# Optimization experiments

Hardware: AMD Instinct MI355X
Metric: run time of the kernel (lower is better)

The kernel has to match this reference:

```python
import jax, jax.numpy as jnp
import numpy as np

STRIDE, PAD, DIL, DG, GROUPS = 1, 1, 1, 1, 1


def setup_inputs() -> dict:
    key = jax.random.key(0)
    k1, k2, k3, k4 = jax.random.split(key, 4)
    B, Cin, H, W = 4, 64, 128, 128
    Cout, kh, kw = 64, 3, 3
    x = jax.random.normal(k1, (B, Cin, H, W), jnp.float32)
    # learned offsets: [B, dg*2*kh*kw, Ho, Wo], interleaved (y, x) per kernel tap
    offset = jax.random.normal(k2, (B, DG * 2 * kh * kw, H, W), jnp.float32)
    # modulation mask: [B, dg*kh*kw, Ho, Wo] in (0,1) (sigmoid applied upstream in DCNv2 packs)
    mask = jax.random.uniform(k3, (B, DG * kh * kw, H, W), jnp.float32)
    stdv = 1.0 / np.sqrt(Cin * kh * kw)
    weight = jax.random.uniform(k4, (Cout, Cin // GROUPS, kh, kw), jnp.float32, -stdv, stdv)
    bias = jnp.zeros((Cout,), jnp.float32)
    return {"x": x, "offset": offset, "mask": mask, "weight": weight, "bias": bias}


def reference(x, offset, mask, weight, bias):
    B, Cin, H, W = x.shape
    Cout, _, kh, kw = weight.shape
    K2 = kh * kw
    Ho = (H + 2 * PAD - DIL * (kh - 1) - 1) // STRIDE + 1
    Wo = (W + 2 * PAD - DIL * (kw - 1) - 1) // STRIDE + 1
    Cg = Cin // DG

    # base sampling grid per kernel tap: [K2, Ho, Wo]
    ky = (jnp.arange(kh) * DIL).repeat(kw)          # [K2]
    kx = jnp.tile(jnp.arange(kw) * DIL, kh)          # [K2]
    base_y = jnp.arange(Ho) * STRIDE - PAD           # [Ho]
    base_x = jnp.arange(Wo) * STRIDE - PAD           # [Wo]
    grid_y = ky[:, None, None] + base_y[None, :, None]  # [K2, Ho, 1]
    grid_x = kx[:, None, None] + base_x[None, None, :]  # [K2, 1, Wo]

    # offsets: [B, dg, K2, 2, Ho, Wo] with channel 0=y, 1=x (DCNv2 interleaving)
    off = offset.reshape(B, DG, K2, 2, Ho, Wo)
    py = grid_y[None, None].astype(x.dtype) + off[:, :, :, 0]  # [B, dg, K2, Ho, Wo]
    px = grid_x[None, None].astype(x.dtype) + off[:, :, :, 1]

    y0 = jnp.floor(py).astype(jnp.int32)
    x0 = jnp.floor(px).astype(jnp.int32)
    ly = py - y0.astype(x.dtype)
    lx = px - x0.astype(x.dtype)

    xg = x.reshape(B, DG, Cg, H * W)

    def gather(iy, ix):
        valid = ((iy >= 0) & (iy < H) & (ix >= 0) & (ix < W)).astype(x.dtype)
        idx = jnp.clip(iy, 0, H - 1) * W + jnp.clip(ix, 0, W - 1)   # [B, dg, K2, Ho, Wo]
        flat = idx.reshape(B, DG, 1, -1)
        vals = jnp.take_along_axis(xg, flat, axis=3)                 # [B, dg, Cg, K2*Ho*Wo]
        return vals.reshape(B, DG, Cg, K2, Ho, Wo) * valid[:, :, None]

    w00 = ((1 - ly) * (1 - lx))[:, :, None]
    w01 = ((1 - ly) * lx)[:, :, None]
    w10 = (ly * (1 - lx))[:, :, None]
    w11 = (ly * lx)[:, :, None]

    sampled = (gather(y0, x0) * w00 + gather(y0, x0 + 1) * w01
               + gather(y0 + 1, x0) * w10 + gather(y0 + 1, x0 + 1) * w11)
    sampled = sampled * mask.reshape(B, DG, 1, K2, Ho, Wo)

    # im2col GEMM (groups=1): [B, Cin*K2, Ho*Wo] x [Cout, Cin*K2]
    cols = sampled.reshape(B, Cin * K2, Ho * Wo)
    wf = weight.reshape(Cout, Cin * K2)
    out = jnp.einsum('ok,bkp->bop', wf, cols).reshape(B, Cout, Ho, Wo)
    return out + bias[None, :, None, None]
```

## Files before the change

### kernel.cpp

```cpp
#include <hip/hip_runtime.h>
#include <math.h>

#define H_    128
#define W_    128
#define HW_   (H_ * W_)
#define CIN_  64
#define COUT_ 64
#define K2_   9
#define B_    4
#define NROWS 10
#define LDS_BYTES (NROWS * 128 * 128)

typedef __bf16 bf16x8 __attribute__((ext_vector_type(8)));
typedef __bf16 bf16x4 __attribute__((ext_vector_type(4)));
typedef float  f32x4  __attribute__((ext_vector_type(4)));

__global__ __launch_bounds__(256) void wtrans3_kernel(const float* __restrict__ w,
                                                      __bf16* __restrict__ wt3) {
    int idx = blockIdx.x * 256 + threadIdx.x;
    if (idx >= K2_ * 2 * 4 * 64 * 8) return;
    int e    = idx & 7;
    int lane = (idx >> 3) & 63;
    int ct   = (idx >> 9) & 3;
    int s    = (idx >> 11) & 1;
    int k    = idx >> 12;
    int co   = ct * 16 + (lane & 15);
    int cin  = s * 32 + (lane >> 4) * 8 + e;
    wt3[idx] = (__bf16)w[(co * CIN_ + cin) * K2_ + k];
}

__global__ __launch_bounds__(1024, 4)
__attribute__((amdgpu_waves_per_eu(4, 4)))
void dcn_lds_kernel(
    const float* __restrict__ x,
    const float* __restrict__ offset,
    const float* __restrict__ mask,
    const __bf16* __restrict__ wt3,
    const float* __restrict__ bias,
    float* __restrict__ out)
{
    extern __shared__ char sm[];

    const int tid  = threadIdx.x;
    const int wave = tid >> 6;
    const int lane = tid & 63;
    const int n16  = lane & 15;
    const int kb   = lane >> 4;

    const int bid0 = blockIdx.x;
    const int bidx = (bid0 & 7) * 32 + (bid0 >> 3);
    const int b   = bidx >> 6;
    const int ho0 = (bidx & 63) * 2;

    const float* xb = x + (size_t)b * CIN_ * HW_;

    {
        const int g5     = tid >> 5;
        const int px4    = tid & 31;
        const int rowpar = g5 >> 4;
        const int c0     = (g5 & 15) * 4;
        const int chunk  = c0 >> 3;
        const int eoff   = (c0 & 7) * 2;
#pragma unroll
        for (int it = 0; it < 5; ++it) {
            const int r = it * 2 + rowpar;
            const int srow = min(max(ho0 - 4 + r, 0), H_ - 1);
            const float* g = xb + ((size_t)c0 * H_ + srow) * W_ + px4 * 4;
            const float4 v0 = *(const float4*)(g);
            const float4 v1 = *(const float4*)(g + HW_);
            const float4 v2 = *(const float4*)(g + 2 * HW_);
            const float4 v3 = *(const float4*)(g + 3 * HW_);
            const float* f0 = (const float*)&v0;
            const float* f1 = (const float*)&v1;
            const float* f2 = (const float*)&v2;
            const float* f3 = (const float*)&v3;
#pragma unroll
            for (int e = 0; e < 4; ++e) {
                const int px = px4 * 4 + e;
                const int q  = (chunk + px + (px >> 3)) & 7;
                bf16x4 pk;
                pk[0] = (__bf16)f0[e];
                pk[1] = (__bf16)f1[e];
                pk[2] = (__bf16)f2[e];
                pk[3] = (__bf16)f3[e];
                *(bf16x4*)(sm + (((size_t)r * 128 + px) * 8 + q) * 16 + eoff) = pk;
            }
        }
    }
    __syncthreads();

    const int rr  = wave >> 3;
    const int til = wave & 7;
    const int ho  = ho0 + rr;
    const int wos = til * 16 + n16;
    const int pix = ho * W_ + wos;
    const float* offb = offset + (size_t)b * (2 * K2_) * HW_ + pix;
    const float* mb   = mask   + (size_t)b * K2_ * HW_ + pix;

    f32x4 acc[4];
#pragma unroll
    for (int t = 0; t < 4; ++t) acc[t] = (f32x4){0.f, 0.f, 0.f, 0.f};

    float oy = offb[0];
    float ox = offb[HW_];
    float mm = mb[0];

#pragma unroll 3
    for (int k = 0; k < K2_; ++k) {
        const int ky = k / 3, kx = k % 3;
        const float py  = (float)(ho - 1 + ky) + oy;
        const float pxf = (float)(wos - 1 + kx) + ox;
        const float fy = floorf(py), fx = floorf(pxf);
        const int   y0 = (int)fy,    x0 = (int)fx;
        const float ly = py - fy,    lx = pxf - fx;

        const float vy0 = (y0 >= 0 && y0 < H_)         ? 1.f : 0.f;
        const float vy1 = (y0 + 1 >= 0 && y0 + 1 < H_) ? 1.f : 0.f;
        const float vx0 = (x0 >= 0 && x0 < W_)         ? 1.f : 0.f;
        const float vx1 = (x0 + 1 >= 0 && x0 + 1 < W_) ? 1.f : 0.f;
        const float W00 = mm * (1.f - ly) * (1.f - lx) * vy0 * vx0;
        const float W01 = mm * (1.f - ly) * lx         * vy0 * vx1;
        const float W10 = mm * ly * (1.f - lx)         * vy1 * vx0;
        const float W11 = mm * ly * lx                 * vy1 * vx1;
        const int cy0 = min(max(y0, 0), H_ - 1);
        const int cy1 = min(max(y0 + 1, 0), H_ - 1);
        const int cx0 = min(max(x0, 0), W_ - 1);
        const int cx1 = min(max(x0 + 1, 0), W_ - 1);

        const int s0 = cy0 - ho0 + 4;
        const int s1 = cy1 - ho0 + 4;
        const bool need0 = ((unsigned)s0 > 9u) && (vy0 != 0.f);
        const bool need1 = ((unsigned)s1 > 9u) && (vy1 != 0.f);
        const int s0c = min(max(s0, 0), 9);
        const int s1c = min(max(s1, 0), 9);
        const int key0 = cx0 + (cx0 >> 3);
        const int key1 = cx1 + (cx1 >> 3);

        const char* r00 = sm + ((size_t)(s0c * 128 + cx0) * 8) * 16;
        const char* r01 = sm + ((size_t)(s0c * 128 + cx1) * 8) * 16;
        const char* r10 = sm + ((size_t)(s1c * 128 + cx0) * 8) * 16;
        const char* r11 = sm + ((size_t)(s1c * 128 + cx1) * 8) * 16;

        bf16x8 a00 = *(const bf16x8*)(r00 + (((kb     + key0) & 7) << 4));
        bf16x8 c00 = *(const bf16x8*)(r00 + (((kb + 4 + key0) & 7) << 4));
        bf16x8 a01 = *(const bf16x8*)(r01 + (((kb     + key1) & 7) << 4));
        bf16x8 c01 = *(const bf16x8*)(r01 + (((kb + 4 + key1) & 7) << 4));
        bf16x8 a10 = *(const bf16x8*)(r10 + (((kb     + key0) & 7) << 4));
        bf16x8 c10 = *(const bf16x8*)(r10 + (((kb + 4 + key0) & 7) << 4));
        bf16x8 a11 = *(const bf16x8*)(r11 + (((kb     + key1) & 7) << 4));
        bf16x8 c11 = *(const bf16x8*)(r11 + (((kb + 4 + key1) & 7) << 4));

        if (__builtin_expect(need0, 0)) {
            const float* gl = xb + (size_t)(kb * 8) * HW_ + (size_t)cy0 * W_;
            const float* gh = gl + (size_t)32 * HW_;
#pragma unroll
            for (int e = 0; e < 8; ++e) {
                a00[e] = (__bf16)gl[(size_t)e * HW_ + cx0];
                a01[e] = (__bf16)gl[(size_t)e * HW_ + cx1];
                c00[e] = (__bf16)gh[(size_t)e * HW_ + cx0];
                c01[e] = (__bf16)gh[(size_t)e * HW_ + cx1];
            }
        }
        if (__builtin_expect(need1, 0)) {
            const float* gl = xb + (size_t)(kb * 8) * HW_ + (size_t)cy1 * W_;
            const float* gh = gl + (size_t)32 * HW_;
#pragma unroll
            for (int e = 0; e < 8; ++e) {
                a10[e] = (__bf16)gl[(size_t)e * HW_ + cx0];
                a11[e] = (__bf16)gl[(size_t)e * HW_ + cx1];
                c10[e] = (__bf16)gh[(size_t)e * HW_ + cx0];
                c11[e] = (__bf16)gh[(size_t)e * HW_ + cx1];
            }
        }

        if (k + 1 < K2_) {
            oy = offb[(2 * (k + 1)) * HW_];
            ox = offb[(2 * (k + 1) + 1) * HW_];
            mm = mb[(k + 1) * HW_];
        }

        bf16x8 bf0, bf1;
#pragma unroll
        for (int e = 0; e < 8; ++e) {
            const float v0 = W00 * (float)a00[e] + W01 * (float)a01[e]
                           + W10 * (float)a10[e] + W11 * (float)a11[e];
            const float v1 = W00 * (float)c00[e] + W01 * (float)c01[e]
                           + W10 * (float)c10[e] + W11 * (float)c11[e];
            bf0[e] = (__bf16)v0;
            bf1[e] = (__bf16)v1;
        }

        const __bf16* wk = wt3 + (size_t)k * (2 * 4 * 64 * 8);
#pragma unroll
        for (int ct = 0; ct < 4; ++ct) {
            const bf16x8 A0 = *(const bf16x8*)(wk + (0 * 4 + ct) * 512 + lane * 8);
            const bf16x8 A1 = *(const bf16x8*)(wk + (1 * 4 + ct) * 512 + lane * 8);
            acc[ct] = __builtin_amdgcn_mfma_f32_16x16x32_bf16(A0, bf0, acc[ct], 0, 0, 0);
            acc[ct] = __builtin_amdgcn_mfma_f32_16x16x32_bf16(A1, bf1, acc[ct], 0, 0, 0);
        }
    }

#pragma unroll
    for (int ct = 0; ct < 4; ++ct) {
#pragma unroll
        for (int r = 0; r < 4; ++r) {
            const int co = ct * 16 + kb * 4 + r;
            out[((size_t)(b * COUT_ + co)) * HW_ + pix] = acc[ct][r] + bias[co];
        }
    }
}

extern "C" void kernel_launch(void* const* d_in, const int* in_sizes, int n_in,
                              void* d_out, int out_size, void* d_ws, size_t ws_size,
                              hipStream_t stream) {
    const float* x      = (const float*)d_in[0];
    const float* offset = (const float*)d_in[1];
    const float* mask   = (const float*)d_in[2];
    const float* weight = (const float*)d_in[3];
    const float* bias   = (const float*)d_in[4];
    float* out = (float*)d_out;
    __bf16* wt3 = (__bf16*)d_ws;

    hipFuncSetAttribute(reinterpret_cast<const void*>(dcn_lds_kernel),
                        hipFuncAttributeMaxDynamicSharedMemorySize, LDS_BYTES);

    wtrans3_kernel<<<(K2_ * 2 * 4 * 64 * 8 + 255) / 256, 256, 0, stream>>>(weight, wt3);
    dcn_lds_kernel<<<B_ * H_ / 2, 1024, LDS_BYTES, stream>>>(x, offset, mask, wt3, bias, out);
}
```

Before: 32.71 us.

## Software-pipeline bilinear sampling one tap ahead of MFMA accumulation

Restructures the tap loop so the LDS corner loads for tap k+1 are issued before tap k's MFMAs, and offset/mask loads are prefetched two taps ahead. The loop is fully unrolled and the interpolation for the next tap is done after the MFMAs. The aim is to hide LDS/global load latency behind matrix math, at the cost of more live registers, which could lower occupancy.

```diff
diff --git a/kernel.cpp b/kernel.cpp
--- a/kernel.cpp
+++ b/kernel.cpp
@@ -101,15 +101,13 @@
 #pragma unroll
     for (int t = 0; t < 4; ++t) acc[t] = (f32x4){0.f, 0.f, 0.f, 0.f};
 
-    float oy = offb[0];
-    float ox = offb[HW_];
-    float mm = mb[0];
-
-#pragma unroll 3
-    for (int k = 0; k < K2_; ++k) {
+    auto sample_corners = [&](int k, float oy_, float ox_, float mm_,
+                              bf16x8& a00, bf16x8& c00, bf16x8& a01, bf16x8& c01,
+                              bf16x8& a10, bf16x8& c10, bf16x8& a11, bf16x8& c11,
+                              float& W00, float& W01, float& W10, float& W11) {
         const int ky = k / 3, kx = k % 3;
-        const float py  = (float)(ho - 1 + ky) + oy;
-        const float pxf = (float)(wos - 1 + kx) + ox;
+        const float py  = (float)(ho - 1 + ky) + oy_;
+        const float pxf = (float)(wos - 1 + kx) + ox_;
         const float fy = floorf(py), fx = floorf(pxf);
         const int   y0 = (int)fy,    x0 = (int)fx;
         const float ly = py - fy,    lx = pxf - fx;
@@ -118,10 +116,10 @@
         const float vy1 = (y0 + 1 >= 0 && y0 + 1 < H_) ? 1.f : 0.f;
         const float vx0 = (x0 >= 0 && x0 < W_)         ? 1.f : 0.f;
         const float vx1 = (x0 + 1 >= 0 && x0 + 1 < W_) ? 1.f : 0.f;
-        const float W00 = mm * (1.f - ly) * (1.f - lx) * vy0 * vx0;
-        const float W01 = mm * (1.f - ly) * lx         * vy0 * vx1;
-        const float W10 = mm * ly * (1.f - lx)         * vy1 * vx0;
-        const float W11 = mm * ly * lx                 * vy1 * vx1;
+        W00 = mm_ * (1.f - ly) * (1.f - lx) * vy0 * vx0;
+        W01 = mm_ * (1.f - ly) * lx         * vy0 * vx1;
+        W10 = mm_ * ly * (1.f - lx)         * vy1 * vx0;
+        W11 = mm_ * ly * lx                 * vy1 * vx1;
         const int cy0 = min(max(y0, 0), H_ - 1);
         const int cy1 = min(max(y0 + 1, 0), H_ - 1);
         const int cx0 = min(max(x0, 0), W_ - 1);
@@ -141,14 +139,14 @@
         const char* r10 = sm + ((size_t)(s1c * 128 + cx0) * 8) * 16;
         const char* r11 = sm + ((size_t)(s1c * 128 + cx1) * 8) * 16;
 
-        bf16x8 a00 = *(const bf16x8*)(r00 + (((kb     + key0) & 7) << 4));
-        bf16x8 c00 = *(const bf16x8*)(r00 + (((kb + 4 + key0) & 7) << 4));
-        bf16x8 a01 = *(const bf16x8*)(r01 + (((kb     + key1) & 7) << 4));
-        bf16x8 c01 = *(const bf16x8*)(r01 + (((kb + 4 + key1) & 7) << 4));
-        bf16x8 a10 = *(const bf16x8*)(r10 + (((kb     + key0) & 7) << 4));
-        bf16x8 c10 = *(const bf16x8*)(r10 + (((kb + 4 + key0) & 7) << 4));
-        bf16x8 a11 = *(const bf16x8*)(r11 + (((kb     + key1) & 7) << 4));
-        bf16x8 c11 = *(const bf16x8*)(r11 + (((kb + 4 + key1) & 7) << 4));
+        a00 = *(const bf16x8*)(r00 + (((kb     + key0) & 7) << 4));
+        c00 = *(const bf16x8*)(r00 + (((kb + 4 + key0) & 7) << 4));
+        a01 = *(const bf16x8*)(r01 + (((kb     + key1) & 7) << 4));
+        c01 = *(const bf16x8*)(r01 + (((kb + 4 + key1) & 7) << 4));
+        a10 = *(const bf16x8*)(r10 + (((kb     + key0) & 7) << 4));
+        c10 = *(const bf16x8*)(r10 + (((kb + 4 + key0) & 7) << 4));
+        a11 = *(const bf16x8*)(r11 + (((kb     + key1) & 7) << 4));
+        c11 = *(const bf16x8*)(r11 + (((kb + 4 + key1) & 7) << 4));
 
         if (__builtin_expect(need0, 0)) {
             const float* gl = xb + (size_t)(kb * 8) * HW_ + (size_t)cy0 * W_;
@@ -172,22 +170,42 @@
                 c11[e] = (__bf16)gh[(size_t)e * HW_ + cx1];
             }
         }
-
+    };
+
+    float oy = offb[0];
+    float ox = offb[HW_];
+    float mm = mb[0];
+
+    bf16x8 bf0, bf1;
+    {
+        bf16x8 a00, c00, a01, c01, a10, c10, a11, c11;
+        float W00, W01, W10, W11;
+        sample_corners(0, oy, ox, mm, a00, c00, a01, c01, a10, c10, a11, c11,
+                       W00, W01, W10, W11);
+#pragma unroll
+        for (int e = 0; e < 8; ++e) {
+            bf0[e] = (__bf16)(W00 * (float)a00[e] + W01 * (float)a01[e]
+                            + W10 * (float)a10[e] + W11 * (float)a11[e]);
+            bf1[e] = (__bf16)(W00 * (float)c00[e] + W01 * (float)c01[e]
+                            + W10 * (float)c10[e] + W11 * (float)c11[e]);
+        }
+    }
+    oy = offb[2 * HW_];
+    ox = offb[3 * HW_];
+    mm = mb[HW_];
+
+#pragma unroll
+    for (int k = 0; k < K2_; ++k) {
+        bf16x8 a00, c00, a01, c01, a10, c10, a11, c11;
+        float W00 = 0.f, W01 = 0.f, W10 = 0.f, W11 = 0.f;
         if (k + 1 < K2_) {
-            oy = offb[(2 * (k + 1)) * HW_];
-            ox = offb[(2 * (k + 1) + 1) * HW_];
-            mm = mb[(k + 1) * HW_];
-        }
-
-        bf16x8 bf0, bf1;
-#pragma unroll
-        for (int e = 0; e < 8; ++e) {
-            const float v0 = W00 * (float)a00[e] + W01 * (float)a01[e]
-                           + W10 * (float)a10[e] + W11 * (float)a11[e];
-            const float v1 = W00 * (float)c00[e] + W01 * (float)c01[e]
-                           + W10 * (float)c10[e] + W11 * (float)c11[e];
-            bf0[e] = (__bf16)v0;
-            bf1[e] = (__bf16)v1;
+            sample_corners(k + 1, oy, ox, mm, a00, c00, a01, c01, a10, c10, a11, c11,
+                           W00, W01, W10, W11);
+        }
+        if (k + 2 < K2_) {
+            oy = offb[(2 * (k + 2)) * HW_];
+            ox = offb[(2 * (k + 2) + 1) * HW_];
+            mm = mb[(k + 2) * HW_];
         }
 
         const __bf16* wk = wt3 + (size_t)k * (2 * 4 * 64 * 8);
@@ -197,6 +215,16 @@
             const bf16x8 A1 = *(const bf16x8*)(wk + (1 * 4 + ct) * 512 + lane * 8);
             acc[ct] = __builtin_amdgcn_mfma_f32_16x16x32_bf16(A0, bf0, acc[ct], 0, 0, 0);
             acc[ct] = __builtin_amdgcn_mfma_f32_16x16x32_bf16(A1, bf1, acc[ct], 0, 0, 0);
+        }
+
+        if (k + 1 < K2_) {
+#pragma unroll
+            for (int e = 0; e < 8; ++e) {
+                bf0[e] = (__bf16)(W00 * (float)a00[e] + W01 * (float)a01[e]
+                                + W10 * (float)a10[e] + W11 * (float)a11[e]);
+                bf1[e] = (__bf16)(W00 * (float)c00[e] + W01 * (float)c01[e]
+                                + W10 * (float)c10[e] + W11 * (float)c11[e]);
+            }
         }
     }
 
```

New measurement: 35.77 us. 1.09x slower.
